# Kernel optimization log

Hardware: AMD Instinct MI355X
Metric: run time of the kernel (lower is better)

The kernel has to match this reference:

```python
import jax, jax.numpy as jnp
import numpy as np

H = 1024      # hidden_size
I = 2048      # expert intermediate_size (SwiGLU)
E = 8         # num_local_experts
B, S = 2, 4096
EPS = 1e-5
INIT = 0.02


def setup_inputs() -> dict:
    key = jax.random.key(0)
    ks = jax.random.split(key, 9)
    return {
        "hidden_states": jax.random.normal(ks[0], (B, S, H), jnp.float32),
        "ln_w": jnp.ones((H,), jnp.float32),
        "ln_b": jnp.zeros((H,), jnp.float32),
        "router_w": jax.random.normal(ks[1], (H, E), jnp.float32) * INIT,
        "gate_w": jax.random.normal(ks[2], (E, H, I), jnp.float32) * INIT,
        "up_w": jax.random.normal(ks[3], (E, H, I), jnp.float32) * INIT,
        "down_w": jax.random.normal(ks[4], (E, I, H), jnp.float32) * INIT,
        "sh_gate": jax.random.normal(ks[5], (H, I), jnp.float32) * INIT,
        "sh_up": jax.random.normal(ks[6], (H, I), jnp.float32) * INIT,
        "sh_down": jax.random.normal(ks[7], (I, H), jnp.float32) * INIT,
    }


def _layernorm(x, w, b):
    mu = jnp.mean(x, axis=-1, keepdims=True)
    var = jnp.mean(jnp.square(x - mu), axis=-1, keepdims=True)
    return (x - mu) * jax.lax.rsqrt(var + EPS) * w + b


def reference(hidden_states, ln_w, ln_b, router_w, gate_w, up_w, down_w,
              sh_gate, sh_up, sh_down):
    b, s, h = hidden_states.shape
    normed = _layernorm(hidden_states, ln_w, ln_b)
    xf = normed.reshape(-1, h)                       # [T, H]

    # Router: top-1 expert per token, sigmoid gating (Llama-4 style)
    logits = xf @ router_w                           # [T, E]
    top_idx = jnp.argmax(logits, axis=-1)            # [T]
    top_score = jax.nn.sigmoid(jnp.max(logits, axis=-1))  # [T]

    # Routed experts: scan over experts, mask+scale tokens assigned to each.
    def body(acc, ew):
        g, u, d, e = ew
        w = jnp.where(top_idx == e, top_score, 0.0)[:, None]  # [T, 1]
        xe = xf * w                                            # gate score applied to input
        hmid = jax.nn.silu(xe @ g) * (xe @ u)                  # [T, I]
        return acc + hmid @ d, None

    routed, _ = jax.lax.scan(
        body, jnp.zeros_like(xf), (gate_w, up_w, down_w, jnp.arange(E)))

    # Shared expert (dense SwiGLU) applied to all tokens
    shared = (jax.nn.silu(xf @ sh_gate) * (xf @ sh_up)) @ sh_down  # [T, H]

    moe_out = (routed + shared).reshape(b, s, h)
    return hidden_states + moe_out
```

## Files before the change

### kernel.cpp

```cpp
#include <hip/hip_runtime.h>

typedef unsigned short ushort_t;
typedef unsigned int uint_t;

#define T_TOK 8192
#define HDIM 1024
#define IDIM 2048
#define NEXP 8
#define RPAD_MAX 10240
#define TOTROWS (RPAD_MAX + T_TOK)

using f32x4 = __attribute__((ext_vector_type(4))) float;
using s16x8 = __attribute__((ext_vector_type(8))) short;

#define SBAR() do { asm volatile("" ::: "memory"); __builtin_amdgcn_s_barrier(); asm volatile("" ::: "memory"); } while (0)
#define VMW(n) asm volatile("s_waitcnt vmcnt(" #n ")" ::: "memory")
#define LGKM(n) do { asm volatile("s_waitcnt lgkmcnt(" #n ")" ::: "memory"); __builtin_amdgcn_sched_barrier(0); } while (0)
#define SCHB() __builtin_amdgcn_sched_barrier(0)

__device__ __forceinline__ float b2f(ushort_t h) {
    return __uint_as_float(((uint_t)h) << 16);
}
__device__ __forceinline__ ushort_t f2bf(float f) {
    uint_t u = __float_as_uint(f);
    uint_t r = (u + 0x7FFFu + ((u >> 16) & 1u)) >> 16;
    return (ushort_t)r;
}
__device__ __forceinline__ void gload16(const void* g, void* l) {
    __builtin_amdgcn_global_load_lds(
        (const __attribute__((address_space(1))) void*)g,
        (__attribute__((address_space(3))) void*)l, 16, 0, 0);
}
__device__ __forceinline__ void sbmap(int bid, int SBC, int NSB, int& rt, int& ct) {
    int x = bid & 7, j = bid >> 3;
    int r = j >> 5, pos = j & 31;
    int sb = r * 8 + x;
    int rem = NSB - r * 8;
    if (rem < 8) {
        int share = 8 / rem;
        int cap = 32 / share;
        sb = r * 8 + x / share;
        pos = (x % share) * cap + (pos % cap);
    }
    int sbr = sb / SBC, sbc = sb % SBC;
    rt = sbr * 4 + (pos >> 3);
    ct = sbc * 8 + (pos & 7);
}

__global__ __launch_bounds__(256) void tcvt64(
    const float* __restrict__ gw, const float* __restrict__ shg,
    const float* __restrict__ uw, const float* __restrict__ shu,
    const float* __restrict__ dw, const float* __restrict__ shd,
    ushort_t* __restrict__ gwt, ushort_t* __restrict__ uwt,
    ushort_t* __restrict__ dwt) {
    __shared__ float tile[64][65];
    int z = blockIdx.z;
    const float* src;
    ushort_t* dst;
    int R, C, bx = blockIdx.x, by = blockIdx.y;
    if (z < 18) {
        int zz = z % 9;
        R = HDIM; C = IDIM;
        if (z < 9) { src = zz < 8 ? gw + (size_t)zz * HDIM * IDIM : shg; dst = gwt + (size_t)zz * IDIM * HDIM; }
        else       { src = zz < 8 ? uw + (size_t)zz * HDIM * IDIM : shu; dst = uwt + (size_t)zz * IDIM * HDIM; }
    } else {
        int zz = z - 18;
        R = IDIM; C = HDIM;
        src = zz < 8 ? dw + (size_t)zz * IDIM * HDIM : shd;
        dst = dwt + (size_t)zz * HDIM * IDIM;
        int t = bx; bx = by; by = t;
    }
    int c0 = bx * 64, r0 = by * 64;
    int t = threadIdx.x;
    int rrow = t >> 4, cg = (t & 15) * 4;
#pragma unroll
    for (int i = 0; i < 4; ++i) {
        int row = rrow + i * 16;
        float4 v = *(const float4*)&src[(size_t)(r0 + row) * C + c0 + cg];
        tile[row][cg] = v.x;
        tile[row][cg + 1] = v.y;
        tile[row][cg + 2] = v.z;
        tile[row][cg + 3] = v.w;
    }
    __syncthreads();
    int cw = t >> 3, rg = (t & 7) * 8;
#pragma unroll
    for (int i = 0; i < 2; ++i) {
        int c = cw + i * 32;
        s16x8 o;
#pragma unroll
        for (int j = 0; j < 8; ++j) o[j] = (short)f2bf(tile[rg + j][c]);
        *(s16x8*)&dst[(size_t)(c0 + c) * R + r0 + rg] = o;
    }
}

__global__ __launch_bounds__(256) void ln_router(
    const float* __restrict__ x, const float* __restrict__ lnw,
    const float* __restrict__ lnb, const float* __restrict__ rw,
    ushort_t* __restrict__ normed, int* __restrict__ top_idx,
    float* __restrict__ top_score, int* __restrict__ cnt) {
    int w = threadIdx.x >> 6, lane = threadIdx.x & 63;
    int t = blockIdx.x * 4 + w;
    const float4* xr = (const float4*)(x + (size_t)t * HDIM);
    float4 v[4];
    float s = 0.f, ss = 0.f;
#pragma unroll
    for (int i = 0; i < 4; ++i) {
        v[i] = xr[lane + i * 64];
        s += v[i].x + v[i].y + v[i].z + v[i].w;
        ss += v[i].x * v[i].x + v[i].y * v[i].y + v[i].z * v[i].z + v[i].w * v[i].w;
    }
#pragma unroll
    for (int m = 32; m; m >>= 1) {
        s += __shfl_xor(s, m);
        ss += __shfl_xor(ss, m);
    }
    float mu = s * (1.f / HDIM);
    float rsg = rsqrtf(ss * (1.f / HDIM) - mu * mu + 1e-5f);
    float lg[8] = {0, 0, 0, 0, 0, 0, 0, 0};
#pragma unroll
    for (int i = 0; i < 4; ++i) {
        int h0 = (lane + i * 64) * 4;
        float4 lw = *(const float4*)&lnw[h0];
        float4 lb = *(const float4*)&lnb[h0];
        float xn0 = (v[i].x - mu) * rsg * lw.x + lb.x;
        float xn1 = (v[i].y - mu) * rsg * lw.y + lb.y;
        float xn2 = (v[i].z - mu) * rsg * lw.z + lb.z;
        float xn3 = (v[i].w - mu) * rsg * lw.w + lb.w;
        ushort4 o;
        o.x = f2bf(xn0); o.y = f2bf(xn1); o.z = f2bf(xn2); o.w = f2bf(xn3);
        *(ushort4*)&normed[(size_t)t * HDIM + h0] = o;
        const float* rp = rw + (size_t)h0 * NEXP;
#pragma unroll
        for (int e = 0; e < 8; ++e)
            lg[e] += xn0 * rp[e] + xn1 * rp[8 + e] + xn2 * rp[16 + e] + xn3 * rp[24 + e];
    }
#pragma unroll
    for (int m = 32; m; m >>= 1)
#pragma unroll
        for (int e = 0; e < 8; ++e) lg[e] += __shfl_xor(lg[e], m);
    if (!lane) {
        float best = -1e30f;
        int bi = 0;
#pragma unroll
        for (int e = 0; e < 8; ++e)
            if (lg[e] > best) { best = lg[e]; bi = e; }
        top_idx[t] = bi;
        top_score[t] = 1.f / (1.f + __expf(-best));
        atomicAdd(&cnt[bi], 1);
    }
}

__global__ void scan_k(const int* __restrict__ cnt, int* __restrict__ pad_off,
                       int* __restrict__ fill) {
    if (threadIdx.x == 0) {
        int o = 0;
        for (int e = 0; e < NEXP; e++) {
            pad_off[e] = o;
            o += (cnt[e] + 255) & ~255;
        }
        pad_off[NEXP] = o;
    }
    if (threadIdx.x < NEXP) fill[threadIdx.x] = 0;
}

__global__ __launch_bounds__(256) void scatter_k(
    const ushort_t* __restrict__ normed, const int* __restrict__ top_idx,
    const float* __restrict__ top_score, const int* __restrict__ pad_off,
    int* __restrict__ fill, int* __restrict__ order, ushort_t* __restrict__ xs) {
    int w = threadIdx.x >> 6, lane = threadIdx.x & 63;
    int t = blockIdx.x * 4 + w;
    int p = 0;
    if (!lane) {
        int e = top_idx[t];
        p = pad_off[e] + atomicAdd(&fill[e], 1);
        order[p] = t;
    }
    p = __shfl(p, 0);
    float sc = top_score[t];
    const s16x8* src = (const s16x8*)(normed + (size_t)t * HDIM);
    s16x8* dst = (s16x8*)(xs + (size_t)p * HDIM);
#pragma unroll
    for (int j = 0; j < 2; ++j) {
        s16x8 a = src[lane + j * 64];
        s16x8 o;
#pragma unroll
        for (int k = 0; k < 8; ++k) o[k] = (short)f2bf(b2f((ushort_t)a[k]) * sc);
        dst[lane + j * 64] = o;
    }
}

__global__ __launch_bounds__(512, 2) void gemm1_k(
    const ushort_t* __restrict__ X, const ushort_t* __restrict__ Wg,
    const ushort_t* __restrict__ Wu, const int* __restrict__ pad_off,
    ushort_t* __restrict__ hmid) {
    __shared__ __align__(16) ushort_t lds[2 * 32768];
    const int CT = IDIM / 128;
    const int NH = HDIM / 64;
    int rt, ct;
    sbmap(blockIdx.x, CT / 8, (TOTROWS / 256 / 4) * (CT / 8), rt, ct);
    int row0 = rt * 256, col0 = ct * 128;
    int e;
    if (row0 >= RPAD_MAX) e = 8;
    else {
        if (row0 >= pad_off[NEXP]) return;
        e = 0;
        while (e < 7 && row0 >= pad_off[e + 1]) ++e;
    }
    const ushort_t* wgp = Wg + (size_t)e * IDIM * HDIM;
    const ushort_t* wup = Wu + (size_t)e * IDIM * HDIM;

    const int tid = threadIdx.x, l = tid & 63, w = tid >> 6;
    const int wm = w >> 2, wn = w & 3;
    const int lr = l & 15, lg4 = l >> 4;

    const ushort_t* sA[4];
#pragma unroll
    for (int j = 0; j < 4; ++j) {
        int gi = tid + j * 512, row = gi >> 3, kg = (gi & 7) ^ (row & 7);
        sA[j] = X + (size_t)(row0 + row) * HDIM + kg * 8;
    }
    const ushort_t *sBg[2], *sBu[2];
#pragma unroll
    for (int j = 0; j < 2; ++j) {
        int gi = tid + j * 512, row = gi >> 3, kg = (gi & 7) ^ (row & 7);
        sBg[j] = wgp + (size_t)(col0 + row) * HDIM + kg * 8;
        sBu[j] = wup + (size_t)(col0 + row) * HDIM + kg * 8;
    }
    const int sl0 = (lg4 ^ (lr & 7)) * 8, sl1 = ((4 + lg4) ^ (lr & 7)) * 8;
    const int aob = (wm * 128 + lr) * 64;
    const int bob = (wn * 32 + lr) * 64;

    f32x4 accg[8][2] = {};
    f32x4 accu[8][2] = {};

#define G1_STAGE(h) do { int ko = (h) * 64; int hb_ = ((h) & 1) * 32768;       \
        gload16(sA[0] + ko, &lds[hb_ + tid * 8]);                              \
        gload16(sA[1] + ko, &lds[hb_ + 4096 + tid * 8]);                       \
        gload16(sA[2] + ko, &lds[hb_ + 8192 + tid * 8]);                       \
        gload16(sA[3] + ko, &lds[hb_ + 12288 + tid * 8]);                      \
        gload16(sBg[0] + ko, &lds[hb_ + 16384 + tid * 8]);                     \
        gload16(sBg[1] + ko, &lds[hb_ + 20480 + tid * 8]);                     \
        gload16(sBu[0] + ko, &lds[hb_ + 24576 + tid * 8]);                     \
        gload16(sBu[1] + ko, &lds[hb_ + 28672 + tid * 8]); } while (0)

#define G1_PH(h, DOSTAGE) do {                                                 \
        const int hb = ((h) & 1) * 32768;                                      \
        s16x8 a0[8], a1[8], b0[4], b1[4];                                      \
        _Pragma("unroll")                                                      \
        for (int m = 0; m < 8; ++m) a0[m] = *(const s16x8*)&lds[hb + aob + m * 1024 + sl0]; \
        _Pragma("unroll")                                                      \
        for (int n = 0; n < 2; ++n) {                                          \
            b0[n] = *(const s16x8*)&lds[hb + 16384 + bob + n * 1024 + sl0];    \
            b0[2 + n] = *(const s16x8*)&lds[hb + 24576 + bob + n * 1024 + sl0]; \
        }                                                                      \
        SCHB();                                                                \
        _Pragma("unroll")                                                      \
        for (int m = 0; m < 8; ++m) a1[m] = *(const s16x8*)&lds[hb + aob + m * 1024 + sl1]; \
        _Pragma("unroll")                                                      \
        for (int n = 0; n < 2; ++n) {                                          \
            b1[n] = *(const s16x8*)&lds[hb + 16384 + bob + n * 1024 + sl1];    \
            b1[2 + n] = *(const s16x8*)&lds[hb + 24576 + bob + n * 1024 + sl1]; \
        }                                                                      \
        SCHB();                                                                \
        if (DOSTAGE) G1_STAGE((h) + 1);                                        \
        LGKM(12);                                                              \
        __builtin_amdgcn_s_setprio(1);                                         \
        _Pragma("unroll")                                                      \
        for (int m = 0; m < 8; ++m) {                                          \
            accg[m][0] = __builtin_amdgcn_mfma_f32_16x16x32_bf16(a0[m], b0[0], accg[m][0], 0, 0, 0); \
            accg[m][1] = __builtin_amdgcn_mfma_f32_16x16x32_bf16(a0[m], b0[1], accg[m][1], 0, 0, 0); \
            accu[m][0] = __builtin_amdgcn_mfma_f32_16x16x32_bf16(a0[m], b0[2], accu[m][0], 0, 0, 0); \
            accu[m][1] = __builtin_amdgcn_mfma_f32_16x16x32_bf16(a0[m], b0[3], accu[m][1], 0, 0, 0); \
        }                                                                      \
        __builtin_amdgcn_s_setprio(0);                                         \
        LGKM(0);                                                               \
        __builtin_amdgcn_s_setprio(1);                                         \
        _Pragma("unroll")                                                      \
        for (int m = 0; m < 8; ++m) {                                          \
            accg[m][0] = __builtin_amdgcn_mfma_f32_16x16x32_bf16(a1[m], b1[0], accg[m][0], 0, 0, 0); \
            accg[m][1] = __builtin_amdgcn_mfma_f32_16x16x32_bf16(a1[m], b1[1], accg[m][1], 0, 0, 0); \
            accu[m][0] = __builtin_amdgcn_mfma_f32_16x16x32_bf16(a1[m], b1[2], accu[m][0], 0, 0, 0); \
            accu[m][1] = __builtin_amdgcn_mfma_f32_16x16x32_bf16(a1[m], b1[3], accu[m][1], 0, 0, 0); \
        }                                                                      \
        __builtin_amdgcn_s_setprio(0);                                         \
        VMW(0);                                                                \
        SBAR();                                                                \
    } while (0)

    G1_STAGE(0);
    VMW(0);
    SBAR();
    for (int h = 0; h < NH - 1; ++h) G1_PH(h, 1);
    G1_PH(NH - 1, 0);

#pragma unroll
    for (int mf = 0; mf < 8; ++mf) {
        int row = row0 + wm * 128 + mf * 16 + lg4 * 4;
#pragma unroll
        for (int nf = 0; nf < 2; ++nf) {
            int col = col0 + wn * 32 + nf * 16 + lr;
#pragma unroll
            for (int rr = 0; rr < 4; ++rr) {
                float g = accg[mf][nf][rr], u = accu[mf][nf][rr];
                float val = g / (1.f + __expf(-g)) * u;
                hmid[(size_t)(row + rr) * IDIM + col] = f2bf(val);
            }
        }
    }
#undef G1_STAGE
#undef G1_PH
}

template <int SHARED>
__global__ __launch_bounds__(512, 2) void gemm2_k(
    const ushort_t* __restrict__ Hm, const ushort_t* __restrict__ Wd,
    const int* __restrict__ pad_off, const int* __restrict__ order,
    const float* __restrict__ hs, float* __restrict__ out, int RT) {
    __shared__ __align__(16) ushort_t lds[2 * 32768];
    const int CT = 4;
    const int NH = IDIM / 64;
    int nwg = RT * CT;
    int bid = blockIdx.x;
    int q = nwg >> 3, r = nwg & 7;
    int xcd = bid & 7, idx = bid >> 3;
    int wg = (xcd < r ? xcd * (q + 1) : r * (q + 1) + (xcd - r) * q) + idx;
    int rt = wg >> 2, ct = wg & 3;
    int row0 = rt * 256, col0 = ct * 256;
    const ushort_t* wdp;
    if (SHARED) {
        wdp = Wd + (size_t)8 * HDIM * IDIM;
    } else {
        if (row0 >= pad_off[NEXP]) return;
        int e = 0;
        while (e < 7 && row0 >= pad_off[e + 1]) ++e;
        wdp = Wd + (size_t)e * HDIM * IDIM;
    }
    const int tid = threadIdx.x, l = tid & 63, w = tid >> 6;
    const int wm = w >> 2, wn = w & 3;
    const int lr = l & 15, lg4 = l >> 4;

    const ushort_t* sA[4];
    const ushort_t* sB[4];
#pragma unroll
    for (int j = 0; j < 4; ++j) {
        int gi = tid + j * 512, row = gi >> 3, kg = (gi & 7) ^ (row & 7);
        sA[j] = Hm + (size_t)(row0 + row) * IDIM + kg * 8;
        sB[j] = wdp + (size_t)(col0 + row) * IDIM + kg * 8;
    }
    const int sl0 = (lg4 ^ (lr & 7)) * 8, sl1 = ((4 + lg4) ^ (lr & 7)) * 8;
    const int aob = (wm * 128 + lr) * 64;
    const int bob = (wn * 64 + lr) * 64;

    f32x4 acc[8][4] = {};

#define G2_STAGE(h) do { int ko = (h) * 64; int hb_ = ((h) & 1) * 32768;       \
        gload16(sA[0] + ko, &lds[hb_ + tid * 8]);                              \
        gload16(sA[1] + ko, &lds[hb_ + 4096 + tid * 8]);                       \
        gload16(sA[2] + ko, &lds[hb_ + 8192 + tid * 8]);                       \
        gload16(sA[3] + ko, &lds[hb_ + 12288 + tid * 8]);                      \
        gload16(sB[0] + ko, &lds[hb_ + 16384 + tid * 8]);                      \
        gload16(sB[1] + ko, &lds[hb_ + 20480 + tid * 8]);                      \
        gload16(sB[2] + ko, &lds[hb_ + 24576 + tid * 8]);                      \
        gload16(sB[3] + ko, &lds[hb_ + 28672 + tid * 8]); } while (0)

#define G2_PH(h, DOSTAGE) do {                                                 \
        const int hb = ((h) & 1) * 32768;                                      \
        s16x8 a0[8], a1[8], b0[4], b1[4];                                      \
        _Pragma("unroll")                                                      \
        for (int m = 0; m < 8; ++m) a0[m] = *(const s16x8*)&lds[hb + aob + m * 1024 + sl0]; \
        _Pragma("unroll")                                                      \
        for (int n = 0; n < 4; ++n) b0[n] = *(const s16x8*)&lds[hb + 16384 + bob + n * 1024 + sl0]; \
        SCHB();                                                                \
        _Pragma("unroll")                                                      \
        for (int m = 0; m < 8; ++m) a1[m] = *(const s16x8*)&lds[hb + aob + m * 1024 + sl1]; \
        _Pragma("unroll")                                                      \
        for (int n = 0; n < 4; ++n) b1[n] = *(const s16x8*)&lds[hb + 16384 + bob + n * 1024 + sl1]; \
        SCHB();                                                                \
        if (DOSTAGE) G2_STAGE((h) + 1);                                        \
        LGKM(12);                                                              \
        __builtin_amdgcn_s_setprio(1);                                         \
        _Pragma("unroll")                                                      \
        for (int m = 0; m < 8; ++m)                                            \
            _Pragma("unroll")                                                  \
            for (int n = 0; n < 4; ++n)                                        \
                acc[m][n] = __builtin_amdgcn_mfma_f32_16x16x32_bf16(a0[m], b0[n], acc[m][n], 0, 0, 0); \
        __builtin_amdgcn_s_setprio(0);                                         \
        LGKM(0);                                                               \
        __builtin_amdgcn_s_setprio(1);                                         \
        _Pragma("unroll")                                                      \
        for (int m = 0; m < 8; ++m)                                            \
            _Pragma("unroll")                                                  \
            for (int n = 0; n < 4; ++n)                                        \
                acc[m][n] = __builtin_amdgcn_mfma_f32_16x16x32_bf16(a1[m], b1[n], acc[m][n], 0, 0, 0); \
        __builtin_amdgcn_s_setprio(0);                                         \
        VMW(0);                                                                \
        SBAR();                                                                \
    } while (0)

    G2_STAGE(0);
    VMW(0);
    SBAR();
    for (int h = 0; h < NH - 1; ++h) G2_PH(h, 1);
    G2_PH(NH - 1, 0);

#pragma unroll
    for (int mf = 0; mf < 8; ++mf) {
        int row = row0 + wm * 128 + mf * 16 + lg4 * 4;
#pragma unroll
        for (int rr = 0; rr < 4; ++rr) {
            int rw_ = row + rr;
            int tok;
            if (SHARED) tok = rw_;
            else { tok = order[rw_]; if (tok < 0) continue; }
            size_t ob = (size_t)tok * HDIM;
#pragma unroll
            for (int nf = 0; nf < 4; ++nf) {
                int col = col0 + wn * 64 + nf * 16 + lr;
                if (SHARED) out[ob + col] += hs[ob + col] + acc[mf][nf][rr];
                else        out[ob + col] = acc[mf][nf][rr];
            }
        }
    }
#undef G2_STAGE
#undef G2_PH
}

extern "C" void kernel_launch(void* const* d_in, const int* in_sizes, int n_in,
                              void* d_out, int out_size, void* d_ws, size_t ws_size,
                              hipStream_t stream) {
    const float* hs = (const float*)d_in[0];
    const float* lnw = (const float*)d_in[1];
    const float* lnb = (const float*)d_in[2];
    const float* rw = (const float*)d_in[3];
    const float* gw = (const float*)d_in[4];
    const float* uw = (const float*)d_in[5];
    const float* dw = (const float*)d_in[6];
    const float* shg = (const float*)d_in[7];
    const float* shu = (const float*)d_in[8];
    const float* shd = (const float*)d_in[9];
    float* out = (float*)d_out;

    char* p = (char*)d_ws;
    auto alloc = [&](size_t bytes) {
        void* r = (void*)p;
        p += (bytes + 255) & ~(size_t)255;
        return r;
    };
    ushort_t* xsbuf = (ushort_t*)alloc((size_t)TOTROWS * HDIM * 2);
    ushort_t* hmid = (ushort_t*)alloc((size_t)TOTROWS * IDIM * 2);
    ushort_t* gwt = (ushort_t*)alloc((size_t)9 * IDIM * HDIM * 2);
    ushort_t* uwt = (ushort_t*)alloc((size_t)9 * IDIM * HDIM * 2);
    ushort_t* dwt = (ushort_t*)alloc((size_t)9 * HDIM * IDIM * 2);
    int* cnt = (int*)alloc(NEXP * 4);
    int* pad_off = (int*)alloc((NEXP + 1) * 4);
    int* fill = (int*)alloc(NEXP * 4);
    int* top_idx = (int*)alloc(T_TOK * 4);
    float* top_sc = (float*)alloc(T_TOK * 4);
    int* order = (int*)alloc(RPAD_MAX * 4);

    ushort_t* normed = xsbuf + (size_t)RPAD_MAX * HDIM;

    hipMemsetAsync(cnt, 0, NEXP * 4, stream);
    hipMemsetAsync(order, 0xFF, RPAD_MAX * 4, stream);
    hipMemsetAsync(xsbuf, 0, (size_t)RPAD_MAX * HDIM * 2, stream);

    tcvt64<<<dim3(IDIM / 64, HDIM / 64, 27), 256, 0, stream>>>(
        gw, shg, uw, shu, dw, shd, gwt, uwt, dwt);

    ln_router<<<T_TOK / 4, 256, 0, stream>>>(hs, lnw, lnb, rw, normed, top_idx, top_sc, cnt);
    scan_k<<<1, 64, 0, stream>>>(cnt, pad_off, fill);
    scatter_k<<<T_TOK / 4, 256, 0, stream>>>(normed, top_idx, top_sc, pad_off, fill, order, xsbuf);

    {
        int RT = TOTROWS / 256, CT = IDIM / 128;
        gemm1_k<<<RT * CT, 512, 0, stream>>>(xsbuf, gwt, uwt, pad_off, hmid);
    }
    {
        int RT = RPAD_MAX / 256;
        gemm2_k<0><<<RT * 4, 512, 0, stream>>>(
            hmid, dwt, pad_off, order, hs, out, RT);
    }
    {
        int RT = T_TOK / 256;
        gemm2_k<1><<<RT * 4, 512, 0, stream>>>(
            hmid + (size_t)RPAD_MAX * IDIM, dwt, pad_off, order, hs, out, RT);
    }
}
```

Measured before the change: 578.3 us.

## Deepen GEMM pipelines to four K=32 LDS stages with a new swizzle

Both expert GEMM kernels now step through K in 32-wide slices instead of 64-wide ones, and the LDS becomes a 4-slot ring buffer. Global-to-LDS loads are issued three stages ahead, and partial vmcnt waits replace the full drain before each barrier. This is meant to hide global memory latency behind the MFMA work. A new row-pair LDS layout and XOR slot swizzle changes how fragments are read. The cost is twice as many barriers per K, and the tail handling and swizzle carry correctness risk.

Result: no change. 588.0 us (+1.7%).

```diff
diff --git a/kernel.cpp b/kernel.cpp
--- a/kernel.cpp
+++ b/kernel.cpp
@@ -30,6 +30,11 @@
     __builtin_amdgcn_global_load_lds(
         (const __attribute__((address_space(1))) void*)g,
         (__attribute__((address_space(3))) void*)l, 16, 0, 0);
+}
+__device__ __forceinline__ void gdec(int gi, int& r, int& kg) {
+    int prow = gi >> 3, v = (gi & 7) ^ (prow & 7);
+    r = 2 * prow + (v >> 2);
+    kg = v & 3;
 }
 __device__ __forceinline__ void sbmap(int bid, int SBC, int NSB, int& rt, int& ct) {
     int x = bid & 7, j = bid >> 3;
@@ -194,9 +199,9 @@
     const ushort_t* __restrict__ X, const ushort_t* __restrict__ Wg,
     const ushort_t* __restrict__ Wu, const int* __restrict__ pad_off,
     ushort_t* __restrict__ hmid) {
-    __shared__ __align__(16) ushort_t lds[2 * 32768];
+    __shared__ __align__(16) ushort_t lds[4 * 16384];
     const int CT = IDIM / 128;
-    const int NH = HDIM / 64;
+    const int NH = HDIM / 32;
     int rt, ct;
     sbmap(blockIdx.x, CT / 8, (TOTROWS / 256 / 4) * (CT / 8), rt, ct);
     int row0 = rt * 256, col0 = ct * 128;
@@ -214,85 +219,75 @@
     const int wm = w >> 2, wn = w & 3;
     const int lr = l & 15, lg4 = l >> 4;
 
-    const ushort_t* sA[4];
-#pragma unroll
-    for (int j = 0; j < 4; ++j) {
-        int gi = tid + j * 512, row = gi >> 3, kg = (gi & 7) ^ (row & 7);
-        sA[j] = X + (size_t)(row0 + row) * HDIM + kg * 8;
-    }
-    const ushort_t *sBg[2], *sBu[2];
-#pragma unroll
-    for (int j = 0; j < 2; ++j) {
-        int gi = tid + j * 512, row = gi >> 3, kg = (gi & 7) ^ (row & 7);
-        sBg[j] = wgp + (size_t)(col0 + row) * HDIM + kg * 8;
-        sBu[j] = wup + (size_t)(col0 + row) * HDIM + kg * 8;
-    }
-    const int sl0 = (lg4 ^ (lr & 7)) * 8, sl1 = ((4 + lg4) ^ (lr & 7)) * 8;
-    const int aob = (wm * 128 + lr) * 64;
-    const int bob = (wn * 32 + lr) * 64;
+    int rA0, kA0, rA1, kA1, rB, kB;
+    gdec(tid, rA0, kA0);
+    gdec(512 + tid, rA1, kA1);
+    gdec(tid, rB, kB);
+    const ushort_t* srcA0 = X + (size_t)(row0 + rA0) * HDIM + kA0 * 8;
+    const ushort_t* srcA1 = X + (size_t)(row0 + rA1) * HDIM + kA1 * 8;
+    const ushort_t* srcBg = wgp + (size_t)(col0 + rB) * HDIM + kB * 8;
+    const ushort_t* srcBu = wup + (size_t)(col0 + rB) * HDIM + kB * 8;
+
+    const int s_slot = (((l & 1) << 2) | lg4) ^ ((l >> 1) & 7);
+    const int aob = (wm * 64 + (lr >> 1)) * 64 + s_slot * 8;
+    const int bob = (wn * 16 + (lr >> 1)) * 64 + s_slot * 8;
 
     f32x4 accg[8][2] = {};
     f32x4 accu[8][2] = {};
 
-#define G1_STAGE(h) do { int ko = (h) * 64; int hb_ = ((h) & 1) * 32768;       \
-        gload16(sA[0] + ko, &lds[hb_ + tid * 8]);                              \
-        gload16(sA[1] + ko, &lds[hb_ + 4096 + tid * 8]);                       \
-        gload16(sA[2] + ko, &lds[hb_ + 8192 + tid * 8]);                       \
-        gload16(sA[3] + ko, &lds[hb_ + 12288 + tid * 8]);                      \
-        gload16(sBg[0] + ko, &lds[hb_ + 16384 + tid * 8]);                     \
-        gload16(sBg[1] + ko, &lds[hb_ + 20480 + tid * 8]);                     \
-        gload16(sBu[0] + ko, &lds[hb_ + 24576 + tid * 8]);                     \
-        gload16(sBu[1] + ko, &lds[hb_ + 28672 + tid * 8]); } while (0)
-
-#define G1_PH(h, DOSTAGE) do {                                                 \
-        const int hb = ((h) & 1) * 32768;                                      \
-        s16x8 a0[8], a1[8], b0[4], b1[4];                                      \
-        _Pragma("unroll")                                                      \
-        for (int m = 0; m < 8; ++m) a0[m] = *(const s16x8*)&lds[hb + aob + m * 1024 + sl0]; \
+#define G1_STAGE(h) do { int ko = (h) * 32; int hb_ = ((h) & 3) * 16384;       \
+        gload16(srcA0 + ko, &lds[hb_ + tid * 8]);                              \
+        gload16(srcA1 + ko, &lds[hb_ + 4096 + tid * 8]);                       \
+        gload16(srcBg + ko, &lds[hb_ + 8192 + tid * 8]);                       \
+        gload16(srcBu + ko, &lds[hb_ + 12288 + tid * 8]); } while (0)
+
+#define G1_PH(h, VMWAIT, DOSTAGE) do {                                         \
+        const int hb = ((h) & 3) * 16384;                                      \
+        s16x8 a[8], bg[2], bu[2];                                              \
+        _Pragma("unroll")                                                      \
+        for (int m = 0; m < 4; ++m) a[m] = *(const s16x8*)&lds[hb + aob + m * 512]; \
         _Pragma("unroll")                                                      \
         for (int n = 0; n < 2; ++n) {                                          \
-            b0[n] = *(const s16x8*)&lds[hb + 16384 + bob + n * 1024 + sl0];    \
-            b0[2 + n] = *(const s16x8*)&lds[hb + 24576 + bob + n * 1024 + sl0]; \
+            bg[n] = *(const s16x8*)&lds[hb + 8192 + bob + n * 512];            \
+            bu[n] = *(const s16x8*)&lds[hb + 12288 + bob + n * 512];           \
         }                                                                      \
+        _Pragma("unroll")                                                      \
+        for (int m = 0; m < 4; ++m) a[4 + m] = *(const s16x8*)&lds[hb + aob + 2048 + m * 512]; \
         SCHB();                                                                \
-        _Pragma("unroll")                                                      \
-        for (int m = 0; m < 8; ++m) a1[m] = *(const s16x8*)&lds[hb + aob + m * 1024 + sl1]; \
-        _Pragma("unroll")                                                      \
-        for (int n = 0; n < 2; ++n) {                                          \
-            b1[n] = *(const s16x8*)&lds[hb + 16384 + bob + n * 1024 + sl1];    \
-            b1[2 + n] = *(const s16x8*)&lds[hb + 24576 + bob + n * 1024 + sl1]; \
-        }                                                                      \
-        SCHB();                                                                \
-        if (DOSTAGE) G1_STAGE((h) + 1);                                        \
-        LGKM(12);                                                              \
+        if (DOSTAGE) G1_STAGE((h) + 3);                                        \
+        LGKM(4);                                                               \
         __builtin_amdgcn_s_setprio(1);                                         \
         _Pragma("unroll")                                                      \
-        for (int m = 0; m < 8; ++m) {                                          \
-            accg[m][0] = __builtin_amdgcn_mfma_f32_16x16x32_bf16(a0[m], b0[0], accg[m][0], 0, 0, 0); \
-            accg[m][1] = __builtin_amdgcn_mfma_f32_16x16x32_bf16(a0[m], b0[1], accg[m][1], 0, 0, 0); \
-            accu[m][0] = __builtin_amdgcn_mfma_f32_16x16x32_bf16(a0[m], b0[2], accu[m][0], 0, 0, 0); \
-            accu[m][1] = __builtin_amdgcn_mfma_f32_16x16x32_bf16(a0[m], b0[3], accu[m][1], 0, 0, 0); \
+        for (int m = 0; m < 4; ++m) {                                          \
+            accg[m][0] = __builtin_amdgcn_mfma_f32_16x16x32_bf16(a[m], bg[0], accg[m][0], 0, 0, 0); \
+            accg[m][1] = __builtin_amdgcn_mfma_f32_16x16x32_bf16(a[m], bg[1], accg[m][1], 0, 0, 0); \
+            accu[m][0] = __builtin_amdgcn_mfma_f32_16x16x32_bf16(a[m], bu[0], accu[m][0], 0, 0, 0); \
+            accu[m][1] = __builtin_amdgcn_mfma_f32_16x16x32_bf16(a[m], bu[1], accu[m][1], 0, 0, 0); \
         }                                                                      \
         __builtin_amdgcn_s_setprio(0);                                         \
         LGKM(0);                                                               \
         __builtin_amdgcn_s_setprio(1);                                         \
         _Pragma("unroll")                                                      \
-        for (int m = 0; m < 8; ++m) {                                          \
-            accg[m][0] = __builtin_amdgcn_mfma_f32_16x16x32_bf16(a1[m], b1[0], accg[m][0], 0, 0, 0); \
-            accg[m][1] = __builtin_amdgcn_mfma_f32_16x16x32_bf16(a1[m], b1[1], accg[m][1], 0, 0, 0); \
-            accu[m][0] = __builtin_amdgcn_mfma_f32_16x16x32_bf16(a1[m], b1[2], accu[m][0], 0, 0, 0); \
-            accu[m][1] = __builtin_amdgcn_mfma_f32_16x16x32_bf16(a1[m], b1[3], accu[m][1], 0, 0, 0); \
+        for (int m = 0; m < 4; ++m) {                                          \
+            accg[4 + m][0] = __builtin_amdgcn_mfma_f32_16x16x32_bf16(a[4 + m], bg[0], accg[4 + m][0], 0, 0, 0); \
+            accg[4 + m][1] = __builtin_amdgcn_mfma_f32_16x16x32_bf16(a[4 + m], bg[1], accg[4 + m][1], 0, 0, 0); \
+            accu[4 + m][0] = __builtin_amdgcn_mfma_f32_16x16x32_bf16(a[4 + m], bu[0], accu[4 + m][0], 0, 0, 0); \
+            accu[4 + m][1] = __builtin_amdgcn_mfma_f32_16x16x32_bf16(a[4 + m], bu[1], accu[4 + m][1], 0, 0, 0); \
         }                                                                      \
         __builtin_amdgcn_s_setprio(0);                                         \
-        VMW(0);                                                                \
+        VMWAIT;                                                                \
         SBAR();                                                                \
     } while (0)
 
     G1_STAGE(0);
-    VMW(0);
+    G1_STAGE(1);
+    G1_STAGE(2);
+    VMW(8);
     SBAR();
-    for (int h = 0; h < NH - 1; ++h) G1_PH(h, 1);
-    G1_PH(NH - 1, 0);
+    for (int h = 0; h < NH - 3; ++h) G1_PH(h, VMW(8), 1);
+    G1_PH(NH - 3, VMW(4), 0);
+    G1_PH(NH - 2, VMW(0), 0);
+    G1_PH(NH - 1, VMW(0), 0);
 
 #pragma unroll
     for (int mf = 0; mf < 8; ++mf) {
@@ -317,9 +312,9 @@
     const ushort_t* __restrict__ Hm, const ushort_t* __restrict__ Wd,
     const int* __restrict__ pad_off, const int* __restrict__ order,
     const float* __restrict__ hs, float* __restrict__ out, int RT) {
-    __shared__ __align__(16) ushort_t lds[2 * 32768];
+    __shared__ __align__(16) ushort_t lds[4 * 16384];
     const int CT = 4;
-    const int NH = IDIM / 64;
+    const int NH = IDIM / 32;
     int nwg = RT * CT;
     int bid = blockIdx.x;
     int q = nwg >> 3, r = nwg & 7;
@@ -340,69 +335,66 @@
     const int wm = w >> 2, wn = w & 3;
     const int lr = l & 15, lg4 = l >> 4;
 
-    const ushort_t* sA[4];
-    const ushort_t* sB[4];
-#pragma unroll
-    for (int j = 0; j < 4; ++j) {
-        int gi = tid + j * 512, row = gi >> 3, kg = (gi & 7) ^ (row & 7);
-        sA[j] = Hm + (size_t)(row0 + row) * IDIM + kg * 8;
-        sB[j] = wdp + (size_t)(col0 + row) * IDIM + kg * 8;
-    }
-    const int sl0 = (lg4 ^ (lr & 7)) * 8, sl1 = ((4 + lg4) ^ (lr & 7)) * 8;
-    const int aob = (wm * 128 + lr) * 64;
-    const int bob = (wn * 64 + lr) * 64;
+    int rA0, kA0, rA1, kA1;
+    gdec(tid, rA0, kA0);
+    gdec(512 + tid, rA1, kA1);
+    const ushort_t* srcA0 = Hm + (size_t)(row0 + rA0) * IDIM + kA0 * 8;
+    const ushort_t* srcA1 = Hm + (size_t)(row0 + rA1) * IDIM + kA1 * 8;
+    const ushort_t* srcB0 = wdp + (size_t)(col0 + rA0) * IDIM + kA0 * 8;
+    const ushort_t* srcB1 = wdp + (size_t)(col0 + rA1) * IDIM + kA1 * 8;
+
+    const int s_slot = (((l & 1) << 2) | lg4) ^ ((l >> 1) & 7);
+    const int aob = (wm * 64 + (lr >> 1)) * 64 + s_slot * 8;
+    const int bob = (wn * 32 + (lr >> 1)) * 64 + s_slot * 8;
 
     f32x4 acc[8][4] = {};
 
-#define G2_STAGE(h) do { int ko = (h) * 64; int hb_ = ((h) & 1) * 32768;       \
-        gload16(sA[0] + ko, &lds[hb_ + tid * 8]);                              \
-        gload16(sA[1] + ko, &lds[hb_ + 4096 + tid * 8]);                       \
-        gload16(sA[2] + ko, &lds[hb_ + 8192 + tid * 8]);                       \
-        gload16(sA[3] + ko, &lds[hb_ + 12288 + tid * 8]);                      \
-        gload16(sB[0] + ko, &lds[hb_ + 16384 + tid * 8]);                      \
-        gload16(sB[1] + ko, &lds[hb_ + 20480 + tid * 8]);                      \
-        gload16(sB[2] + ko, &lds[hb_ + 24576 + tid * 8]);                      \
-        gload16(sB[3] + ko, &lds[hb_ + 28672 + tid * 8]); } while (0)
-
-#define G2_PH(h, DOSTAGE) do {                                                 \
-        const int hb = ((h) & 1) * 32768;                                      \
-        s16x8 a0[8], a1[8], b0[4], b1[4];                                      \
-        _Pragma("unroll")                                                      \
-        for (int m = 0; m < 8; ++m) a0[m] = *(const s16x8*)&lds[hb + aob + m * 1024 + sl0]; \
-        _Pragma("unroll")                                                      \
-        for (int n = 0; n < 4; ++n) b0[n] = *(const s16x8*)&lds[hb + 16384 + bob + n * 1024 + sl0]; \
+#define G2_STAGE(h) do { int ko = (h) * 32; int hb_ = ((h) & 3) * 16384;       \
+        gload16(srcA0 + ko, &lds[hb_ + tid * 8]);                              \
+        gload16(srcA1 + ko, &lds[hb_ + 4096 + tid * 8]);                       \
+        gload16(srcB0 + ko, &lds[hb_ + 8192 + tid * 8]);                       \
+        gload16(srcB1 + ko, &lds[hb_ + 12288 + tid * 8]); } while (0)
+
+#define G2_PH(h, VMWAIT, DOSTAGE) do {                                         \
+        const int hb = ((h) & 3) * 16384;                                      \
+        s16x8 a[8], b[4];                                                      \
+        _Pragma("unroll")                                                      \
+        for (int m = 0; m < 4; ++m) a[m] = *(const s16x8*)&lds[hb + aob + m * 512]; \
+        _Pragma("unroll")                                                      \
+        for (int n = 0; n < 4; ++n) b[n] = *(const s16x8*)&lds[hb + 8192 + bob + n * 512]; \
+        _Pragma("unroll")                                                      \
+        for (int m = 0; m < 4; ++m) a[4 + m] = *(const s16x8*)&lds[hb + aob + 2048 + m * 512]; \
         SCHB();                                                                \
-        _Pragma("unroll")                                                      \
-        for (int m = 0; m < 8; ++m) a1[m] = *(const s16x8*)&lds[hb + aob + m * 1024 + sl1]; \
-        _Pragma("unroll")                                                      \
-        for (int n = 0; n < 4; ++n) b1[n] = *(const s16x8*)&lds[hb + 16384 + bob + n * 1024 + sl1]; \
-        SCHB();                                                                \
-        if (DOSTAGE) G2_STAGE((h) + 1);                                        \
-        LGKM(12);                                                              \
+        if (DOSTAGE) G2_STAGE((h) + 3);                                        \
+        LGKM(4);                                                               \
         __builtin_amdgcn_s_setprio(1);                                         \
         _Pragma("unroll")                                                      \
-        for (int m = 0; m < 8; ++m)                                            \
+        for (int m = 0; m < 4; ++m)                                            \
             _Pragma("unroll")                                                  \
             for (int n = 0; n < 4; ++n)                                        \
-                acc[m][n] = __builtin_amdgcn_mfma_f32_16x16x32_bf16(a0[m], b0[n], acc[m][n], 0, 0, 0); \
+                acc[m][n] = __builtin_amdgcn_mfma_f32_16x16x32_bf16(a[m], b[n], acc[m][n], 0, 0, 0); \
         __builtin_amdgcn_s_setprio(0);                                         \
         LGKM(0);                                                               \
         __builtin_amdgcn_s_setprio(1);                                         \
         _Pragma("unroll")                                                      \
-        for (int m = 0; m < 8; ++m)                                            \
+        for (int m = 0; m < 4; ++m)                                            \
             _Pragma("unroll")                                                  \
             for (int n = 0; n < 4; ++n)                                        \
-                acc[m][n] = __builtin_amdgcn_mfma_f32_16x16x32_bf16(a1[m], b1[n], acc[m][n], 0, 0, 0); \
+                acc[4 + m][n] = __builtin_amdgcn_mfma_f32_16x16x32_bf16(a[4 + m], b[n], acc[4 + m][n], 0, 0, 0); \
         __builtin_amdgcn_s_setprio(0);                                         \
-        VMW(0);                                                                \
+        VMWAIT;                                                                \
         SBAR();                                                                \
     } while (0)
 
     G2_STAGE(0);
-    VMW(0);
+    G2_STAGE(1);
+    G2_STAGE(2);
+    VMW(8);
     SBAR();
-    for (int h = 0; h < NH - 1; ++h) G2_PH(h, 1);
-    G2_PH(NH - 1, 0);
+    for (int h = 0; h < NH - 3; ++h) G2_PH(h, VMW(8), 1);
+    G2_PH(NH - 3, VMW(4), 0);
+    G2_PH(NH - 2, VMW(0), 0);
+    G2_PH(NH - 1, VMW(0), 0);
 
 #pragma unroll
     for (int mf = 0; mf < 8; ++mf) {
```

## Merge routed and shared down-proj GEMMs into one split-K launch with atomics

Applied to the files above, without the earlier changes.

Fuses the two down-projection launches (routed experts and shared expert) into a single 576-block grid and splits K into two halves, so each block does half the reduction and accumulates into the output with atomicAdd. The output is zeroed with a memset first, and the residual is added only by the first K-half of the shared segment. This aims to fill the GPU better (320 plus 256 blocks instead of two smaller sequential launches) and drop a launch boundary, at the cost of fp32 atomic traffic, an extra output memset and non-deterministic summation order. A helper gdec is added but never used.

New measurement: 628.1 us. 1.09x slower.

```diff
diff --git a/kernel.cpp b/kernel.cpp
--- a/kernel.cpp
+++ b/kernel.cpp
@@ -30,6 +30,11 @@
     __builtin_amdgcn_global_load_lds(
         (const __attribute__((address_space(1))) void*)g,
         (__attribute__((address_space(3))) void*)l, 16, 0, 0);
+}
+__device__ __forceinline__ void gdec(int gi, int& r, int& kg) {
+    int prow = gi >> 3, v = (gi & 7) ^ (prow & 7);
+    r = 2 * prow + (v >> 2);
+    kg = v & 3;
 }
 __device__ __forceinline__ void sbmap(int bid, int SBC, int NSB, int& rt, int& ct) {
     int x = bid & 7, j = bid >> 3;
@@ -312,28 +317,28 @@
 #undef G1_PH
 }
 
-template <int SHARED>
 __global__ __launch_bounds__(512, 2) void gemm2_k(
     const ushort_t* __restrict__ Hm, const ushort_t* __restrict__ Wd,
     const int* __restrict__ pad_off, const int* __restrict__ order,
-    const float* __restrict__ hs, float* __restrict__ out, int RT) {
+    const float* __restrict__ hs, float* __restrict__ out) {
     __shared__ __align__(16) ushort_t lds[2 * 32768];
-    const int CT = 4;
-    const int NH = IDIM / 64;
-    int nwg = RT * CT;
+    const int NH = 16;
     int bid = blockIdx.x;
-    int q = nwg >> 3, r = nwg & 7;
-    int xcd = bid & 7, idx = bid >> 3;
-    int wg = (xcd < r ? xcd * (q + 1) : r * (q + 1) + (xcd - r) * q) + idx;
-    int rt = wg >> 2, ct = wg & 3;
-    int row0 = rt * 256, col0 = ct * 256;
+    int wg = (bid & 7) * 72 + (bid >> 3);
+    int seg = wg >= 320;
+    int id = seg ? wg - 320 : wg;
+    int ct = id & 3, kh = (id >> 2) & 1, rt = id >> 3;
+    int row0 = rt * 256, col0 = ct * 256, k0 = kh * 1024;
+    const ushort_t* A;
     const ushort_t* wdp;
-    if (SHARED) {
+    if (seg) {
+        A = Hm + (size_t)RPAD_MAX * IDIM;
         wdp = Wd + (size_t)8 * HDIM * IDIM;
     } else {
         if (row0 >= pad_off[NEXP]) return;
         int e = 0;
         while (e < 7 && row0 >= pad_off[e + 1]) ++e;
+        A = Hm;
         wdp = Wd + (size_t)e * HDIM * IDIM;
     }
     const int tid = threadIdx.x, l = tid & 63, w = tid >> 6;
@@ -345,8 +350,8 @@
 #pragma unroll
     for (int j = 0; j < 4; ++j) {
         int gi = tid + j * 512, row = gi >> 3, kg = (gi & 7) ^ (row & 7);
-        sA[j] = Hm + (size_t)(row0 + row) * IDIM + kg * 8;
-        sB[j] = wdp + (size_t)(col0 + row) * IDIM + kg * 8;
+        sA[j] = A + (size_t)(row0 + row) * IDIM + k0 + kg * 8;
+        sB[j] = wdp + (size_t)(col0 + row) * IDIM + k0 + kg * 8;
     }
     const int sl0 = (lg4 ^ (lr & 7)) * 8, sl1 = ((4 + lg4) ^ (lr & 7)) * 8;
     const int aob = (wm * 128 + lr) * 64;
@@ -411,14 +416,15 @@
         for (int rr = 0; rr < 4; ++rr) {
             int rw_ = row + rr;
             int tok;
-            if (SHARED) tok = rw_;
+            if (seg) tok = rw_;
             else { tok = order[rw_]; if (tok < 0) continue; }
             size_t ob = (size_t)tok * HDIM;
 #pragma unroll
             for (int nf = 0; nf < 4; ++nf) {
                 int col = col0 + wn * 64 + nf * 16 + lr;
-                if (SHARED) out[ob + col] += hs[ob + col] + acc[mf][nf][rr];
-                else        out[ob + col] = acc[mf][nf][rr];
+                float v = acc[mf][nf][rr];
+                if (seg && kh == 0) v += hs[ob + col];
+                atomicAdd(&out[ob + col], v);
             }
         }
     }
@@ -464,6 +470,7 @@
     hipMemsetAsync(cnt, 0, NEXP * 4, stream);
     hipMemsetAsync(order, 0xFF, RPAD_MAX * 4, stream);
     hipMemsetAsync(xsbuf, 0, (size_t)RPAD_MAX * HDIM * 2, stream);
+    hipMemsetAsync(out, 0, (size_t)T_TOK * HDIM * 4, stream);
 
     tcvt64<<<dim3(IDIM / 64, HDIM / 64, 27), 256, 0, stream>>>(
         gw, shg, uw, shu, dw, shd, gwt, uwt, dwt);
@@ -476,14 +483,5 @@
         int RT = TOTROWS / 256, CT = IDIM / 128;
         gemm1_k<<<RT * CT, 512, 0, stream>>>(xsbuf, gwt, uwt, pad_off, hmid);
     }
-    {
-        int RT = RPAD_MAX / 256;
-        gemm2_k<0><<<RT * 4, 512, 0, stream>>>(
-            hmid, dwt, pad_off, order, hs, out, RT);
-    }
-    {
-        int RT = T_TOK / 256;
-        gemm2_k<1><<<RT * 4, 512, 0, stream>>>(
-            hmid + (size_t)RPAD_MAX * IDIM, dwt, pad_off, order, hs, out, RT);
-    }
-}
+    gemm2_k<<<576, 512, 0, stream>>>(hmid, dwt, pad_off, order, hs, out);
+}
```
